# Optimization experiments

Hardware: AMD Instinct MI355X
Metric: run time of the kernel (lower is better)

The kernel has to match this reference:

```python
import jax, jax.numpy as jnp
import numpy as np

BN_EPS = 1e-5
NUM_GRAPHS = 64


def setup_inputs() -> dict:
    key = jax.random.key(0)
    ks = jax.random.split(key, 10)
    N, F, H, E = 50000, 128, 256, 800000
    x = jax.random.normal(ks[0], (N, F), dtype=jnp.float32)
    edge_index = jax.random.randint(ks[1], (2, E), 0, N, dtype=jnp.int64)
    batch = jnp.sort(jax.random.randint(ks[2], (N,), 0, NUM_GRAPHS, dtype=jnp.int64))
    # Linear weights stored as [in, out]; y = z @ w + b (equivalent to torch Linear)
    w1_0 = jax.random.normal(ks[3], (F, H), dtype=jnp.float32) / np.sqrt(F)
    b1_0 = jnp.zeros((H,), jnp.float32)
    w2_0 = jax.random.normal(ks[4], (H, H), dtype=jnp.float32) / np.sqrt(H)
    b2_0 = jnp.zeros((H,), jnp.float32)
    g_0 = jnp.ones((H,), jnp.float32)
    be_0 = jnp.zeros((H,), jnp.float32)
    w1_r = jax.random.normal(ks[5], (3, H, H), dtype=jnp.float32) / np.sqrt(H)
    b1_r = jnp.zeros((3, H), jnp.float32)
    w2_r = jax.random.normal(ks[6], (3, H, H), dtype=jnp.float32) / np.sqrt(H)
    b2_r = jnp.zeros((3, H), jnp.float32)
    g_r = jnp.ones((3, H), jnp.float32)
    be_r = jnp.zeros((3, H), jnp.float32)
    return dict(x=x, edge_index=edge_index, batch=batch,
                w1_0=w1_0, b1_0=b1_0, w2_0=w2_0, b2_0=b2_0, g_0=g_0, be_0=be_0,
                w1_r=w1_r, b1_r=b1_r, w2_r=w2_r, b2_r=b2_r, g_r=g_r, be_r=be_r)


def _gin_layer(h, src, dst, n, w1, b1, w2, b2, g, be):
    # GINConv with eps=0: MLP(h_i + sum_{j->i} h_j), scatter-add over edges
    agg = jax.ops.segment_sum(h[src], dst, num_segments=n)  # [N, d]
    z = agg + h
    z = jnp.maximum(z @ w1 + b1, 0.0)
    z = z @ w2 + b2
    # BatchNorm1d over the node dimension (training-mode batch statistics)
    mu = jnp.mean(z, axis=0)
    var = jnp.var(z, axis=0)
    z = (z - mu) * jax.lax.rsqrt(var + BN_EPS) * g + be
    return jnp.maximum(z, 0.0)  # ReLU; dropout is identity in eval mode


def reference(x, edge_index, batch, w1_0, b1_0, w2_0, b2_0, g_0, be_0,
              w1_r, b1_r, w2_r, b2_r, g_r, be_r):
    src, dst = edge_index[0], edge_index[1]
    n = x.shape[0]
    h = _gin_layer(x, src, dst, n, w1_0, b1_0, w2_0, b2_0, g_0, be_0)
    for i in range(3):
        h = _gin_layer(h, src, dst, n, w1_r[i], b1_r[i], w2_r[i], b2_r[i], g_r[i], be_r[i])
    # global mean pool per graph id
    counts = jax.ops.segment_sum(jnp.ones((n,), h.dtype), batch, num_segments=NUM_GRAPHS)
    pooled = jax.ops.segment_sum(h, batch, num_segments=NUM_GRAPHS)
    return pooled / jnp.maximum(counts, 1.0)[:, None]
```

## Files before the change

kernel.cpp:

```cpp
#include <hip/hip_runtime.h>

typedef float  f32x4 __attribute__((ext_vector_type(4)));
typedef _Float16 half8 __attribute__((ext_vector_type(8)));

#define BN_EPS 1e-5f
#define NGRAPH 64

struct PrepArgs {
    const float* src[8];
    _Float16*    dst[8];
    int          K[8];
};

__global__ void prep_weights(PrepArgs a) {
    int m = blockIdx.y;
    int K = a.K[m];
    int total = K << 8;
    int idx = blockIdx.x * blockDim.x + threadIdx.x;
    if (idx >= total) return;
    int n = idx / K;
    int k = idx - n * K;
    a.dst[m][idx] = (_Float16)a.src[m][(size_t)k * 256 + n];
}

__global__ void cast_x(const float* __restrict__ x, _Float16* __restrict__ o, int total) {
    int i = (blockIdx.x * blockDim.x + threadIdx.x) << 3;
    if (i >= total) return;
    f32x4 a = *(const f32x4*)(x + i);
    f32x4 b = *(const f32x4*)(x + i + 4);
    half8 r;
#pragma unroll
    for (int k = 0; k < 4; ++k) { r[k] = (_Float16)a[k]; r[k + 4] = (_Float16)b[k]; }
    *(half8*)(o + i) = r;
}

__global__ void edge_count(const int* __restrict__ ei, int* __restrict__ cnt,
                           int* __restrict__ rank, int E) {
    int e = blockIdx.x * blockDim.x + threadIdx.x;
    if (e < E) rank[e] = atomicAdd(&cnt[ei[E + e]], 1);
}

__global__ void scan_p1(const int* __restrict__ cnt, int* __restrict__ part, int N) {
    __shared__ int lds[256];
    int idx = blockIdx.x * 256 + threadIdx.x;
    lds[threadIdx.x] = (idx < N) ? cnt[idx] : 0;
    __syncthreads();
    for (int d = 128; d > 0; d >>= 1) {
        if (threadIdx.x < d) lds[threadIdx.x] += lds[threadIdx.x + d];
        __syncthreads();
    }
    if (threadIdx.x == 0) part[blockIdx.x] = lds[0];
}

__global__ void scan_p2(int* __restrict__ part, int* __restrict__ off, int N, int nb) {
    __shared__ int lds[256];
    int t = threadIdx.x;
    int v = (t < nb) ? part[t] : 0;
    lds[t] = v;
    __syncthreads();
    for (int d = 1; d < 256; d <<= 1) {
        int a = (t >= d) ? lds[t - d] : 0;
        __syncthreads();
        lds[t] += a;
        __syncthreads();
    }
    if (t < nb) part[t] = lds[t] - v;
    if (t == nb - 1) off[N] = lds[t];
}

__global__ void scan_p3(const int* __restrict__ cnt, const int* __restrict__ part,
                        int* __restrict__ off, int N) {
    __shared__ int lds[256];
    int t = threadIdx.x;
    int idx = blockIdx.x * 256 + t;
    int v = (idx < N) ? cnt[idx] : 0;
    lds[t] = v;
    __syncthreads();
    for (int d = 1; d < 256; d <<= 1) {
        int a = (t >= d) ? lds[t - d] : 0;
        __syncthreads();
        lds[t] += a;
        __syncthreads();
    }
    if (idx < N) off[idx] = part[blockIdx.x] + lds[t] - v;
}

__global__ void edge_fill(const int* __restrict__ ei, const int* __restrict__ off,
                          const int* __restrict__ rank, int* __restrict__ csr_src, int E) {
    int e = blockIdx.x * blockDim.x + threadIdx.x;
    if (e >= E) return;
    csr_src[off[ei[E + e]] + rank[e]] = ei[e];
}

__global__ void bn_coef(const float* __restrict__ stats, const float* __restrict__ gam,
                        const float* __restrict__ bet, _Float16* __restrict__ c16,
                        float* __restrict__ c32, float invN) {
    int c = threadIdx.x;
    float mu = stats[c] * invN;
    float var = stats[256 + c] * invN - mu * mu;
    float s = gam[c] * rsqrtf(var + BN_EPS);
    float t = bet[c] - mu * s;
    c16[c] = (_Float16)s; c16[256 + c] = (_Float16)t;
    c32[c] = s; c32[256 + c] = t;
}

__global__ void gather0(const _Float16* __restrict__ x, const int* __restrict__ off,
                        const int* __restrict__ srcs, _Float16* __restrict__ out, int N) {
    int wid = (blockIdx.x << 2) + (threadIdx.x >> 6);
    if (wid >= N) return;
    int lane = threadIdx.x & 63;
    int q = lane >> 4;
    int fb = (lane & 15) << 3;
    const char* xb = (const char*)x;
    unsigned fb2 = (unsigned)fb << 1;
    float acc[8] = {0.f, 0.f, 0.f, 0.f, 0.f, 0.f, 0.f, 0.f};
    int end = off[wid + 1];
    int e = off[wid] + q;
    for (; e + 4 < end; e += 8) {
        half8 v0 = *(const half8*)(xb + (((unsigned)srcs[e] << 8) + fb2));
        half8 v1 = *(const half8*)(xb + (((unsigned)srcs[e + 4] << 8) + fb2));
        half8 p = v0 + v1;
#pragma unroll
        for (int k = 0; k < 8; ++k) acc[k] += (float)p[k];
    }
    if (e < end) {
        half8 v0 = *(const half8*)(xb + (((unsigned)srcs[e] << 8) + fb2));
#pragma unroll
        for (int k = 0; k < 8; ++k) acc[k] += (float)v0[k];
    }
    if (q == 0) {
        half8 v = *(const half8*)(xb + (((unsigned)wid << 8) + fb2));
#pragma unroll
        for (int k = 0; k < 8; ++k) acc[k] += (float)v[k];
    }
#pragma unroll
    for (int k = 0; k < 8; ++k) {
        acc[k] += __shfl_xor(acc[k], 16);
        acc[k] += __shfl_xor(acc[k], 32);
    }
    if (q == 0) {
        half8 o;
#pragma unroll
        for (int k = 0; k < 8; ++k) o[k] = (_Float16)acc[k];
        *(half8*)(out + (size_t)wid * 128 + fb) = o;
    }
}

__global__ void gather_fused(const _Float16* __restrict__ z, const int* __restrict__ off,
                             const int* __restrict__ srcs, const _Float16* __restrict__ coef,
                             _Float16* __restrict__ out, int N) {
    int wid = (blockIdx.x << 2) + (threadIdx.x >> 6);
    if (wid >= N) return;
    int lane = threadIdx.x & 63;
    int hf = lane >> 5;
    int fb = (lane & 31) << 3;
    half8 sc8 = *(const half8*)(coef + fb);
    half8 tc8 = *(const half8*)(coef + 256 + fb);
    const half8 zero8 = {0, 0, 0, 0, 0, 0, 0, 0};
    const char* zb = (const char*)z;
    unsigned fb2 = (unsigned)fb << 1;
    float acc[8] = {0.f, 0.f, 0.f, 0.f, 0.f, 0.f, 0.f, 0.f};
    int end = off[wid + 1];
    int e = off[wid] + hf;
    for (; e + 6 < end; e += 8) {
        half8 v0 = *(const half8*)(zb + (((unsigned)srcs[e] << 9) + fb2));
        half8 v1 = *(const half8*)(zb + (((unsigned)srcs[e + 2] << 9) + fb2));
        half8 v2 = *(const half8*)(zb + (((unsigned)srcs[e + 4] << 9) + fb2));
        half8 v3 = *(const half8*)(zb + (((unsigned)srcs[e + 6] << 9) + fb2));
        half8 r0 = __builtin_elementwise_max(v0 * sc8 + tc8, zero8);
        half8 r1 = __builtin_elementwise_max(v1 * sc8 + tc8, zero8);
        half8 r2 = __builtin_elementwise_max(v2 * sc8 + tc8, zero8);
        half8 r3 = __builtin_elementwise_max(v3 * sc8 + tc8, zero8);
        half8 p01 = r0 + r1;
        half8 p23 = r2 + r3;
#pragma unroll
        for (int k = 0; k < 8; ++k)
            acc[k] += (float)p01[k] + (float)p23[k];
    }
    for (; e < end; e += 2) {
        half8 v0 = *(const half8*)(zb + (((unsigned)srcs[e] << 9) + fb2));
        half8 r0 = __builtin_elementwise_max(v0 * sc8 + tc8, zero8);
#pragma unroll
        for (int k = 0; k < 8; ++k) acc[k] += (float)r0[k];
    }
    if (hf == 0) {
        half8 v = *(const half8*)(zb + (((unsigned)wid << 9) + fb2));
        half8 r = __builtin_elementwise_max(v * sc8 + tc8, zero8);
#pragma unroll
        for (int k = 0; k < 8; ++k) acc[k] += (float)r[k];
    }
#pragma unroll
    for (int k = 0; k < 8; ++k) acc[k] += __shfl_xor(acc[k], 32);
    if (hf == 0) {
        half8 o;
#pragma unroll
        for (int k = 0; k < 8; ++k) o[k] = (_Float16)acc[k];
        *(half8*)(out + (size_t)wid * 256 + fb) = o;
    }
}

template <int K, int WITH_STATS>
__global__ __launch_bounds__(512, 4) void gemm_kernel(
    const _Float16* __restrict__ A, const _Float16* __restrict__ BT,
    const float* __restrict__ bias, _Float16* __restrict__ Y,
    float* __restrict__ stats, int M) {
    extern __shared__ _Float16 blds[];
    float* sred = (float*)(blds + 17408);
    const int tid = threadIdx.x;
    const int lane = tid & 63, wave = tid >> 6;
    const int i = lane & 15, g = lane >> 4;
    const int rowbase = blockIdx.x * 128 + wave * 16;
    const int arow = min(rowbase + i, M - 1);

    half8 afrag[K / 32];
#pragma unroll
    for (int s = 0; s < K / 32; ++s)
        afrag[s] = *(const half8*)(A + (size_t)arow * K + s * 32 + g * 8);

    f32x4 acc[16];
#pragma unroll
    for (int t = 0; t < 16; ++t) acc[t] = (f32x4){0.f, 0.f, 0.f, 0.f};

    const int scol = tid >> 1;
    const int shalf = (tid & 1) * 32;
    const int ssw = (scol & 7) << 3;
    const int swi = (i & 7) << 3;

#pragma unroll
    for (int kc = 0; kc < K / 64; ++kc) {
        if (kc) __syncthreads();
        {
            const _Float16* src = BT + (size_t)scol * K + kc * 64 + shalf;
            _Float16* dst = blds + scol * 64;
#pragma unroll
            for (int c = 0; c < 32; c += 8)
                *(half8*)(dst + ((shalf + c) ^ ssw)) = *(const half8*)(src + c);
        }
        __syncthreads();
#pragma unroll
        for (int ks = 0; ks < 2; ++ks)
#pragma unroll
            for (int t = 0; t < 16; ++t) {
                half8 b = *(const half8*)(blds + (t * 16 + i) * 64 + ((ks * 32 + g * 8) ^ swi));
                acc[t] = __builtin_amdgcn_mfma_f32_16x16x32_f16(afrag[kc * 2 + ks], b, acc[t], 0, 0, 0);
            }
    }

    const int rg = g * 4;
    if (WITH_STATS) {
#pragma unroll
        for (int t = 0; t < 16; ++t) {
            int c = t * 16 + i;
            float bv = bias[c];
            float s1 = 0.f, s2 = 0.f;
#pragma unroll
            for (int j = 0; j < 4; ++j) {
                if (rowbase + rg + j < M) {
                    float v = acc[t][j] + bv;
                    s1 += v;
                    s2 += v * v;
                }
            }
            s1 += __shfl_xor(s1, 16); s1 += __shfl_xor(s1, 32);
            s2 += __shfl_xor(s2, 16); s2 += __shfl_xor(s2, 32);
            if (g == 0) {
                sred[wave * 256 + c] = s1;
                sred[2048 + wave * 256 + c] = s2;
            }
        }
    }
    __syncthreads();
    if (WITH_STATS) {
        int which = tid >> 8, c = tid & 255;
        float s = 0.f;
#pragma unroll
        for (int w = 0; w < 8; ++w) s += sred[which * 2048 + w * 256 + c];
        atomicAdd(&stats[which * 256 + c], s);
    }

    _Float16* ostage = blds;
#pragma unroll
    for (int ph = 0; ph < 2; ++ph) {
        if (ph) __syncthreads();
#pragma unroll
        for (int tt = 0; tt < 8; ++tt) {
            int t = ph * 8 + tt;
            int lc = tt * 16 + i;
            float bv = bias[t * 16 + i];
#pragma unroll
            for (int j = 0; j < 4; ++j) {
                float v = acc[t][j] + bv;
                if (WITH_STATS == 0) v = fmaxf(v, 0.f);
                ostage[(wave * 16 + rg + j) * 136 + lc] = (_Float16)v;
            }
        }
        __syncthreads();
#pragma unroll
        for (int k = 0; k < 4; ++k) {
            int ch = k * 512 + tid;
            int rl = ch >> 4, pc = (ch & 15) << 3;
            int r = blockIdx.x * 128 + rl;
            if (r < M)
                *(half8*)(Y + (size_t)r * 256 + ph * 128 + pc) =
                    *(const half8*)(ostage + rl * 136 + pc);
        }
    }
}

__global__ void graph_bounds(const int* __restrict__ batch, int* __restrict__ gstart, int N) {
    int t = threadIdx.x;
    if (t > NGRAPH) return;
    if (t == NGRAPH) { gstart[t] = N; return; }
    int lo = 0, hi = N;
    while (lo < hi) { int m = (lo + hi) >> 1; if (batch[m] < t) lo = m + 1; else hi = m; }
    gstart[t] = lo;
}

#define PCHUNK 256
__global__ void pool_stage1(const _Float16* __restrict__ z, const int* __restrict__ batch,
                            const int* __restrict__ gstart, const float* __restrict__ c32,
                            float* __restrict__ acc, int N) {
    __shared__ float lds[8 * 512];
    int c0 = blockIdx.x * PCHUNK;
    int cend = min(c0 + PCHUNK, N);
    int tid = threadIdx.x;
    int rowlane = tid >> 5;
    int fb = (tid & 31) << 3;
    float sc[8], tc[8];
#pragma unroll
    for (int k = 0; k < 8; ++k) { sc[k] = c32[fb + k]; tc[k] = c32[256 + fb + k]; }
    int segs = c0;
    while (segs < cend) {
        int g = batch[segs];
        int sege = min(gstart[g + 1], cend);
        float a[8] = {0.f, 0.f, 0.f, 0.f, 0.f, 0.f, 0.f, 0.f};
        for (int r = segs + rowlane; r < sege; r += 16) {
            half8 v = *(const half8*)(z + (size_t)r * 256 + fb);
#pragma unroll
            for (int k = 0; k < 8; ++k)
                a[k] += fmaxf(fmaf((float)v[k], sc[k], tc[k]), 0.f);
        }
#pragma unroll
        for (int k = 0; k < 8; ++k) lds[k * 512 + tid] = a[k];
        __syncthreads();
#pragma unroll
        for (int d = 8; d > 0; d >>= 1) {
            if (rowlane < d) {
#pragma unroll
                for (int k = 0; k < 8; ++k)
                    lds[k * 512 + tid] += lds[k * 512 + tid + d * 32];
            }
            __syncthreads();
        }
        if (rowlane == 0) {
#pragma unroll
            for (int k = 0; k < 8; ++k)
                atomicAdd(&acc[g * 256 + fb + k], lds[k * 512 + tid]);
        }
        __syncthreads();
        segs = sege;
    }
}

__global__ void pool_finalize(const float* __restrict__ acc, const int* __restrict__ gstart,
                              float* __restrict__ out) {
    int i = blockIdx.x * 256 + threadIdx.x;
    int g = i >> 8;
    int c = gstart[g + 1] - gstart[g];
    out[i] = acc[i] / (float)(c > 0 ? c : 1);
}

extern "C" void kernel_launch(void* const* d_in, const int* in_sizes, int n_in,
                              void* d_out, int out_size, void* d_ws, size_t ws_size,
                              hipStream_t stream) {
    const float* x    = (const float*)d_in[0];
    const int*   ei   = (const int*)d_in[1];
    const int*   batch= (const int*)d_in[2];
    const float* w1_0 = (const float*)d_in[3];
    const float* b1_0 = (const float*)d_in[4];
    const float* w2_0 = (const float*)d_in[5];
    const float* b2_0 = (const float*)d_in[6];
    const float* g_0  = (const float*)d_in[7];
    const float* be_0 = (const float*)d_in[8];
    const float* w1_r = (const float*)d_in[9];
    const float* b1_r = (const float*)d_in[10];
    const float* w2_r = (const float*)d_in[11];
    const float* b2_r = (const float*)d_in[12];
    const float* g_r  = (const float*)d_in[13];
    const float* be_r = (const float*)d_in[14];

    const int N = in_sizes[0] / 128;
    const int E = in_sizes[1] / 2;

    char* p = (char*)d_ws;
    auto alloc = [&](size_t bytes) { char* r = p; p += (bytes + 255) & ~(size_t)255; return r; };
    float*    stats   = (float*)alloc(4 * 512 * sizeof(float));
    _Float16* coef16  = (_Float16*)alloc(512 * sizeof(_Float16));
    float*    coef32  = (float*)alloc(512 * sizeof(float));
    int*      part    = (int*)alloc(256 * sizeof(int));
    int*      off     = (int*)alloc((size_t)(N + 1) * sizeof(int));
    int*      cnt     = (int*)alloc((size_t)N * sizeof(int));
    int*      gstart  = (int*)alloc(65 * sizeof(int));
    float*    accp    = (float*)alloc(NGRAPH * 256 * sizeof(float));
    int*      rank    = (int*)alloc((size_t)E * sizeof(int));
    int*      csr_src = (int*)alloc((size_t)E * sizeof(int));
    _Float16* wT      = (_Float16*)alloc((size_t)491520 * sizeof(_Float16));
    _Float16* x16     = (_Float16*)alloc((size_t)N * 128 * sizeof(_Float16));
    _Float16* zin     = (_Float16*)alloc((size_t)N * 256 * sizeof(_Float16));
    _Float16* y       = (_Float16*)alloc((size_t)N * 256 * sizeof(_Float16));
    _Float16* z       = (_Float16*)alloc((size_t)N * 256 * sizeof(_Float16));

    hipMemsetAsync(stats, 0, 4 * 512 * sizeof(float), stream);
    hipMemsetAsync(cnt, 0, (size_t)N * sizeof(int), stream);
    hipMemsetAsync(accp, 0, NGRAPH * 256 * sizeof(float), stream);

    PrepArgs pa;
    pa.src[0] = w1_0;  pa.dst[0] = wT;           pa.K[0] = 128;
    pa.src[1] = w2_0;  pa.dst[1] = wT + 32768;   pa.K[1] = 256;
    for (int i = 0; i < 3; ++i) {
        pa.src[2 + i] = w1_r + (size_t)i * 65536; pa.dst[2 + i] = wT + 98304 + (size_t)i * 65536; pa.K[2 + i] = 256;
        pa.src[5 + i] = w2_r + (size_t)i * 65536; pa.dst[5 + i] = wT + 294912 + (size_t)i * 65536; pa.K[5 + i] = 256;
    }
    prep_weights<<<dim3(256, 8), 256, 0, stream>>>(pa);
    cast_x<<<(N * 128 / 8 + 255) / 256, 256, 0, stream>>>(x, x16, N * 128);

    const int eb = (E + 255) / 256;
    const int nb = (N + 255) / 256;
    edge_count<<<eb, 256, 0, stream>>>(ei, cnt, rank, E);
    scan_p1<<<nb, 256, 0, stream>>>(cnt, part, N);
    scan_p2<<<1, 256, 0, stream>>>(part, off, N, nb);
    scan_p3<<<nb, 256, 0, stream>>>(cnt, part, off, N);
    edge_fill<<<eb, 256, 0, stream>>>(ei, off, rank, csr_src, E);
    graph_bounds<<<1, 128, 0, stream>>>(batch, gstart, N);

    const int gwb = (N + 3) / 4;
    const int gemmg = (N + 127) / 128;
    const int ldsb = 51200;
    const float invN = 1.0f / (float)N;

    gather0<<<gwb, 256, 0, stream>>>(x16, off, csr_src, zin, N);
    gemm_kernel<128, 0><<<gemmg, 512, ldsb, stream>>>(zin, wT, b1_0, y, nullptr, N);
    gemm_kernel<256, 1><<<gemmg, 512, ldsb, stream>>>(y, wT + 32768, b2_0, z, stats, N);
    bn_coef<<<1, 256, 0, stream>>>(stats, g_0, be_0, coef16, coef32, invN);

    for (int i = 0; i < 3; ++i) {
        gather_fused<<<gwb, 256, 0, stream>>>(z, off, csr_src, coef16, zin, N);
        gemm_kernel<256, 0><<<gemmg, 512, ldsb, stream>>>(
            zin, wT + 98304 + (size_t)i * 65536, b1_r + i * 256, y, nullptr, N);
        gemm_kernel<256, 1><<<gemmg, 512, ldsb, stream>>>(
            y, wT + 294912 + (size_t)i * 65536, b2_r + i * 256, z, stats + (i + 1) * 512, N);
        bn_coef<<<1, 256, 0, stream>>>(stats + (i + 1) * 512, g_r + i * 256, be_r + i * 256,
                                       coef16, coef32, invN);
    }

    pool_stage1<<<(N + PCHUNK - 1) / PCHUNK, 512, 0, stream>>>(
        z, batch, gstart, coef32, accp, N);
    pool_finalize<<<NGRAPH, 256, 0, stream>>>(accp, gstart, (float*)d_out);
}
```

Baseline: 475.6 us.

## Fuse the two MLP GEMMs per layer into one kernel via LDS intermediate

```diff
diff --git a/kernel.cpp b/kernel.cpp
--- a/kernel.cpp
+++ b/kernel.cpp
@@ -199,86 +199,127 @@
     }
 }
 
-template <int K, int WITH_STATS>
-__global__ __launch_bounds__(512, 4) void gemm_kernel(
-    const _Float16* __restrict__ A, const _Float16* __restrict__ BT,
-    const float* __restrict__ bias, _Float16* __restrict__ Y,
+template <int K1>
+__global__ __launch_bounds__(256, 2) void mlp2(
+    const _Float16* __restrict__ A, const _Float16* __restrict__ W1T,
+    const float* __restrict__ b1, const _Float16* __restrict__ W2T,
+    const float* __restrict__ b2, _Float16* __restrict__ Z,
     float* __restrict__ stats, int M) {
-    extern __shared__ _Float16 blds[];
-    float* sred = (float*)(blds + 17408);
+    extern __shared__ _Float16 lds[];
+    _Float16* Wr = lds;
+    _Float16* Yr = lds + 16384;
+    float* sred = (float*)(lds + 32768);
     const int tid = threadIdx.x;
     const int lane = tid & 63, wave = tid >> 6;
     const int i = lane & 15, g = lane >> 4;
-    const int rowbase = blockIdx.x * 128 + wave * 16;
+    const int rowbase = blockIdx.x * 64 + wave * 16;
     const int arow = min(rowbase + i, M - 1);
-
-    half8 afrag[K / 32];
-#pragma unroll
-    for (int s = 0; s < K / 32; ++s)
-        afrag[s] = *(const half8*)(A + (size_t)arow * K + s * 32 + g * 8);
+    const int swi = (i & 7) << 3;
+    const int ssw = (tid & 7) << 3;
+
+    half8 af[K1 / 32];
+#pragma unroll
+    for (int s = 0; s < K1 / 32; ++s)
+        af[s] = *(const half8*)(A + (size_t)arow * K1 + s * 32 + g * 8);
 
     f32x4 acc[16];
 #pragma unroll
     for (int t = 0; t < 16; ++t) acc[t] = (f32x4){0.f, 0.f, 0.f, 0.f};
 
-    const int scol = tid >> 1;
-    const int shalf = (tid & 1) * 32;
-    const int ssw = (scol & 7) << 3;
-    const int swi = (i & 7) << 3;
-
-#pragma unroll
-    for (int kc = 0; kc < K / 64; ++kc) {
+#pragma unroll
+    for (int kc = 0; kc < K1 / 64; ++kc) {
         if (kc) __syncthreads();
         {
-            const _Float16* src = BT + (size_t)scol * K + kc * 64 + shalf;
-            _Float16* dst = blds + scol * 64;
-#pragma unroll
-            for (int c = 0; c < 32; c += 8)
-                *(half8*)(dst + ((shalf + c) ^ ssw)) = *(const half8*)(src + c);
+            const _Float16* src = W1T + (size_t)tid * K1 + kc * 64;
+            _Float16* dst = Wr + tid * 64;
+#pragma unroll
+            for (int c = 0; c < 64; c += 8)
+                *(half8*)(dst + (c ^ ssw)) = *(const half8*)(src + c);
         }
         __syncthreads();
 #pragma unroll
         for (int ks = 0; ks < 2; ++ks)
 #pragma unroll
             for (int t = 0; t < 16; ++t) {
-                half8 b = *(const half8*)(blds + (t * 16 + i) * 64 + ((ks * 32 + g * 8) ^ swi));
-                acc[t] = __builtin_amdgcn_mfma_f32_16x16x32_f16(afrag[kc * 2 + ks], b, acc[t], 0, 0, 0);
+                half8 b = *(const half8*)(Wr + (t * 16 + i) * 64 + ((ks * 32 + g * 8) ^ swi));
+                acc[t] = __builtin_amdgcn_mfma_f32_16x16x32_f16(af[kc * 2 + ks], b, acc[t], 0, 0, 0);
             }
     }
 
     const int rg = g * 4;
-    if (WITH_STATS) {
-#pragma unroll
-        for (int t = 0; t < 16; ++t) {
-            int c = t * 16 + i;
-            float bv = bias[c];
-            float s1 = 0.f, s2 = 0.f;
-#pragma unroll
-            for (int j = 0; j < 4; ++j) {
-                if (rowbase + rg + j < M) {
-                    float v = acc[t][j] + bv;
-                    s1 += v;
-                    s2 += v * v;
-                }
+#pragma unroll
+    for (int t = 0; t < 16; ++t) {
+        int c = t * 16 + i;
+        float bv = b1[c];
+#pragma unroll
+        for (int j = 0; j < 4; ++j) {
+            int r = wave * 16 + rg + j;
+            Yr[r * 256 + (c ^ ((r & 7) << 3))] = (_Float16)fmaxf(acc[t][j] + bv, 0.f);
+        }
+    }
+    __syncthreads();
+
+    half8 af2[8];
+#pragma unroll
+    for (int s = 0; s < 8; ++s)
+        af2[s] = *(const half8*)(Yr + (wave * 16 + i) * 256 + ((s * 32 + g * 8) ^ swi));
+
+#pragma unroll
+    for (int t = 0; t < 16; ++t) acc[t] = (f32x4){0.f, 0.f, 0.f, 0.f};
+
+#pragma unroll
+    for (int kc = 0; kc < 4; ++kc) {
+        if (kc) __syncthreads();
+        {
+            const _Float16* src = W2T + (size_t)tid * 256 + kc * 64;
+            _Float16* dst = Wr + tid * 64;
+#pragma unroll
+            for (int c = 0; c < 64; c += 8)
+                *(half8*)(dst + (c ^ ssw)) = *(const half8*)(src + c);
+        }
+        __syncthreads();
+#pragma unroll
+        for (int ks = 0; ks < 2; ++ks)
+#pragma unroll
+            for (int t = 0; t < 16; ++t) {
+                half8 b = *(const half8*)(Wr + (t * 16 + i) * 64 + ((ks * 32 + g * 8) ^ swi));
+                acc[t] = __builtin_amdgcn_mfma_f32_16x16x32_f16(af2[kc * 2 + ks], b, acc[t], 0, 0, 0);
             }
-            s1 += __shfl_xor(s1, 16); s1 += __shfl_xor(s1, 32);
-            s2 += __shfl_xor(s2, 16); s2 += __shfl_xor(s2, 32);
-            if (g == 0) {
-                sred[wave * 256 + c] = s1;
-                sred[2048 + wave * 256 + c] = s2;
+    }
+
+#pragma unroll
+    for (int t = 0; t < 16; ++t) {
+        int c = t * 16 + i;
+        float bv = b2[c];
+        float s1 = 0.f, s2 = 0.f;
+#pragma unroll
+        for (int j = 0; j < 4; ++j) {
+            if (rowbase + rg + j < M) {
+                float v = acc[t][j] + bv;
+                s1 += v;
+                s2 += v * v;
             }
         }
+        s1 += __shfl_xor(s1, 16); s1 += __shfl_xor(s1, 32);
+        s2 += __shfl_xor(s2, 16); s2 += __shfl_xor(s2, 32);
+        if (g == 0) {
+            sred[wave * 256 + c] = s1;
+            sred[1024 + wave * 256 + c] = s2;
+        }
     }
     __syncthreads();
-    if (WITH_STATS) {
-        int which = tid >> 8, c = tid & 255;
-        float s = 0.f;
-#pragma unroll
-        for (int w = 0; w < 8; ++w) s += sred[which * 2048 + w * 256 + c];
-        atomicAdd(&stats[which * 256 + c], s);
-    }
-
-    _Float16* ostage = blds;
+    {
+        float ss1 = 0.f, ss2 = 0.f;
+#pragma unroll
+        for (int w = 0; w < 4; ++w) {
+            ss1 += sred[w * 256 + tid];
+            ss2 += sred[1024 + w * 256 + tid];
+        }
+        atomicAdd(&stats[tid], ss1);
+        atomicAdd(&stats[256 + tid], ss2);
+    }
+
+    _Float16* ostage = lds;
 #pragma unroll
     for (int ph = 0; ph < 2; ++ph) {
         if (ph) __syncthreads();
@@ -286,22 +327,19 @@
         for (int tt = 0; tt < 8; ++tt) {
             int t = ph * 8 + tt;
             int lc = tt * 16 + i;
-            float bv = bias[t * 16 + i];
-#pragma unroll
-            for (int j = 0; j < 4; ++j) {
-                float v = acc[t][j] + bv;
-                if (WITH_STATS == 0) v = fmaxf(v, 0.f);
-                ostage[(wave * 16 + rg + j) * 136 + lc] = (_Float16)v;
-            }
+            float bv = b2[t * 16 + i];
+#pragma unroll
+            for (int j = 0; j < 4; ++j)
+                ostage[(wave * 16 + rg + j) * 136 + lc] = (_Float16)(acc[t][j] + bv);
         }
         __syncthreads();
 #pragma unroll
         for (int k = 0; k < 4; ++k) {
-            int ch = k * 512 + tid;
+            int ch = k * 256 + tid;
             int rl = ch >> 4, pc = (ch & 15) << 3;
-            int r = blockIdx.x * 128 + rl;
+            int r = blockIdx.x * 64 + rl;
             if (r < M)
-                *(half8*)(Y + (size_t)r * 256 + ph * 128 + pc) =
+                *(half8*)(Z + (size_t)r * 256 + ph * 128 + pc) =
                     *(const half8*)(ostage + rl * 136 + pc);
         }
     }
@@ -407,7 +445,6 @@
     _Float16* wT      = (_Float16*)alloc((size_t)491520 * sizeof(_Float16));
     _Float16* x16     = (_Float16*)alloc((size_t)N * 128 * sizeof(_Float16));
     _Float16* zin     = (_Float16*)alloc((size_t)N * 256 * sizeof(_Float16));
-    _Float16* y       = (_Float16*)alloc((size_t)N * 256 * sizeof(_Float16));
     _Float16* z       = (_Float16*)alloc((size_t)N * 256 * sizeof(_Float16));
 
     hipMemsetAsync(stats, 0, 4 * 512 * sizeof(float), stream);
@@ -433,22 +470,20 @@
     edge_fill<<<eb, 256, 0, stream>>>(ei, off, rank, csr_src, E);
     graph_bounds<<<1, 128, 0, stream>>>(batch, gstart, N);
 
-    const int gwb = (N + 3) / 4;
-    const int gemmg = (N + 127) / 128;
-    const int ldsb = 51200;
+    const int gwb  = (N + 3) / 4;
+    const int mlpg = (N + 63) / 64;
+    const int ldsm = 73728;
     const float invN = 1.0f / (float)N;
 
     gather0<<<gwb, 256, 0, stream>>>(x16, off, csr_src, zin, N);
-    gemm_kernel<128, 0><<<gemmg, 512, ldsb, stream>>>(zin, wT, b1_0, y, nullptr, N);
-    gemm_kernel<256, 1><<<gemmg, 512, ldsb, stream>>>(y, wT + 32768, b2_0, z, stats, N);
+    mlp2<128><<<mlpg, 256, ldsm, stream>>>(zin, wT, b1_0, wT + 32768, b2_0, z, stats, N);
     bn_coef<<<1, 256, 0, stream>>>(stats, g_0, be_0, coef16, coef32, invN);
 
     for (int i = 0; i < 3; ++i) {
         gather_fused<<<gwb, 256, 0, stream>>>(z, off, csr_src, coef16, zin, N);
-        gemm_kernel<256, 0><<<gemmg, 512, ldsb, stream>>>(
-            zin, wT + 98304 + (size_t)i * 65536, b1_r + i * 256, y, nullptr, N);
-        gemm_kernel<256, 1><<<gemmg, 512, ldsb, stream>>>(
-            y, wT + 294912 + (size_t)i * 65536, b2_r + i * 256, z, stats + (i + 1) * 512, N);
+        mlp2<256><<<mlpg, 256, ldsm, stream>>>(
+            zin, wT + 98304 + (size_t)i * 65536, b1_r + i * 256,
+            wT + 294912 + (size_t)i * 65536, b2_r + i * 256, z, stats + (i + 1) * 512, N);
         bn_coef<<<1, 256, 0, stream>>>(stats + (i + 1) * 512, g_r + i * 256, be_r + i * 256,
                                        coef16, coef32, invN);
     }
```

Result: slower. 579.0 us (+21.7%).
